# Optimization experiments

Hardware: AMD Instinct MI355X
Metric: run time of the kernel (lower is better)

The kernel has to match this reference:

```python
import jax, jax.numpy as jnp
import numpy as np

# Module hyperparameters (defaults from OrdinalPeakedCELoss.__init__)
K = 9
ALPHA = 0.4
W_FAR = 7.0
DELTA_FAR = 0.15
W_TAIL = 9.0
TAIL_POWER = 3
W_LPEAK = 12.0
PROB_MARGIN = 0.35
W_EMD = 1.2
CE_WEIGHT = 1.0
EPS = 1e-8
INV_LOGK = float(1.0 / np.log(K))
WIDTHS = np.array([3, 7, 10, 10, 10, 10, 10, 10, 25], dtype=np.float32)


def setup_inputs() -> dict:
    key = jax.random.key(0)
    k1, k2 = jax.random.split(key)
    B = 4_194_304
    logits = jax.random.normal(k1, (B, K), dtype=jnp.float32)
    y = jax.random.randint(k2, (B,), 0, K, dtype=jnp.int32)
    return {"logits": logits, "y": y}


def _loss(logits, y):
    # constant tables (tiny, [K,K])
    classes = jnp.arange(K, dtype=logits.dtype)
    d_idx = jnp.abs(classes[None, :] - classes[:, None])           # [K,K]
    tail_weights = jnp.where(d_idx > 1, (d_idx - 1.0) ** TAIL_POWER, 0.0)
    widths = jnp.asarray(WIDTHS, dtype=logits.dtype)
    cdf_weights = widths / widths.sum()                            # [K]

    # CE (class_weights are all ones -> plain NLL mean), normalized by log K
    logp = jax.nn.log_softmax(logits, axis=1)                      # [B,K]
    nll = -jnp.take_along_axis(logp, y[:, None], axis=1)[:, 0]     # [B]
    ce_loss = nll.mean() * INV_LOGK * CE_WEIGHT

    # probs: softmax, clamp_min(eps), renormalize
    probs = jax.nn.softmax(logits, axis=1)
    probs = jnp.maximum(probs, EPS)
    probs = probs / probs.sum(axis=1, keepdims=True)               # [B,K]

    py = jnp.take_along_axis(probs, y[:, None], axis=1)[:, 0]      # [B]

    # FarProbMargin: max prob among classes with |k-y|>1
    far_mask = d_idx[y] > 1                                        # [B,K]
    far_vals = jnp.where(far_mask, probs, -jnp.inf)
    far_max = jnp.max(far_vals, axis=1)
    far_max = jnp.where(jnp.isfinite(far_max), far_max, 0.0)
    far_margin = jax.nn.relu(far_max - (py - DELTA_FAR)).mean()

    # TailWeighted
    tail = (probs * tail_weights[y]).sum(axis=1).mean()            # [B] -> scalar

    # LocalPeak: neighbors y-1 / y+1 (0 when out of range)
    yl = jnp.clip(y - 1, 0, K - 1)
    yr = jnp.clip(y + 1, 0, K - 1)
    py_left = jnp.where(y > 0, jnp.take_along_axis(probs, yl[:, None], axis=1)[:, 0], 0.0)
    py_right = jnp.where(y + 1 < K, jnp.take_along_axis(probs, yr[:, None], axis=1)[:, 0], 0.0)
    neighbor_max = jnp.maximum(py_left, py_right)
    local_peak = jax.nn.relu(neighbor_max - (py - PROB_MARGIN)).mean()

    # EMD^2 over weighted CDFs
    cdf_pred = jnp.cumsum(probs, axis=1)                           # [B,K]
    cdf_true = (jnp.arange(K)[None, :] <= y[:, None]).astype(probs.dtype)
    emd2 = (((cdf_pred - cdf_true) ** 2) * cdf_weights).sum(axis=1).mean()

    ord_block = W_FAR * far_margin + W_TAIL * tail + W_LPEAK * local_peak + W_EMD * emd2
    return ce_loss + ALPHA * ord_block


def reference(logits, y):
    return _loss(logits, y)
```

## Files before the change

kernel.cpp:

```cpp
#include <hip/hip_runtime.h>
#include <math.h>

#define KC 9
#define BLOCK 256
#define RPT 512
#define NBLOCKS 2048

__device__ __forceinline__ float row_loss(const float x[KC], int yv) {
    constexpr float ALPHA = 0.4f;
    constexpr float W_FAR = 7.0f;
    constexpr float DELTA_FAR = 0.15f;
    constexpr float W_TAIL = 9.0f;
    constexpr float W_LPEAK = 12.0f;
    constexpr float PROB_MARGIN = 0.35f;
    constexpr float INV_LOGK = 0.45511961331341866f;
    constexpr float w[KC] = {3.0f/105.0f, 7.0f/105.0f, 10.0f/105.0f, 10.0f/105.0f,
                             10.0f/105.0f, 10.0f/105.0f, 10.0f/105.0f, 10.0f/105.0f,
                             25.0f/105.0f};

    float e[KC];
    float s = 0.0f;
    #pragma unroll
    for (int k = 0; k < KC; ++k) { e[k] = __expf(x[k]); s += e[k]; }
    const float inv_s = __frcp_rn(s);

    float xy = 0.0f;
    #pragma unroll
    for (int k = 0; k < KC; ++k) xy = (k == yv) ? x[k] : xy;
    const float nll = __logf(s) - xy;

    float p[KC];
    #pragma unroll
    for (int k = 0; k < KC; ++k) p[k] = e[k] * inv_s;

    float py = 0.0f, pl = 0.0f, pr = 0.0f, far_max = 0.0f, tail = 0.0f;
    float cdf = 0.0f, emd = 0.0f;
    #pragma unroll
    for (int k = 0; k < KC; ++k) {
        const int d = k - yv;
        const int ad = (d < 0) ? -d : d;
        py = (d == 0) ? p[k] : py;
        pl = (d == -1) ? p[k] : pl;
        pr = (d == 1) ? p[k] : pr;
        if (ad > 1) {
            far_max = fmaxf(far_max, p[k]);
            const float dm = (float)(ad - 1);
            tail = fmaf(p[k], dm * dm * dm, tail);
        }
        cdf += p[k];
        const float tt = (k <= yv) ? 1.0f : 0.0f;
        const float dlt = cdf - tt;
        emd = fmaf(dlt * dlt, w[k], emd);
    }

    const float far_margin = fmaxf(far_max - (py - DELTA_FAR), 0.0f);
    const float local_peak = fmaxf(fmaxf(pl, pr) - (py - PROB_MARGIN), 0.0f);

    return nll * INV_LOGK +
           ALPHA * (W_FAR * far_margin + W_TAIL * tail +
                    W_LPEAK * local_peak + 1.2f * emd);
}

__global__ __launch_bounds__(BLOCK) void ordinal_loss_kernel(
    const float* __restrict__ logits, const int* __restrict__ y,
    float* __restrict__ partials, int B, float invB)
{
    __shared__ float lds[RPT * KC];
    __shared__ float wave_sums[BLOCK / 64];

    const int t = threadIdx.x;
    const int ntiles = (B + RPT - 1) / RPT;

    float acc = 0.0f;

    for (int tile = blockIdx.x; tile < ntiles; tile += gridDim.x) {
        const int base = tile * RPT;
        const int nrows = (B - base < RPT) ? (B - base) : RPT;
        const int nflt = nrows * KC;
        const float* src = logits + (size_t)base * KC;

        const int y0 = (t < nrows) ? y[base + t] : 0;
        const int y1 = (t + BLOCK < nrows) ? y[base + t + BLOCK] : 0;

        if (nflt == RPT * KC) {
            const float4* src4 = reinterpret_cast<const float4*>(src);
            float4* lds4 = reinterpret_cast<float4*>(lds);
            lds4[t]       = src4[t];
            lds4[t + 256] = src4[t + 256];
            lds4[t + 512] = src4[t + 512];
            lds4[t + 768] = src4[t + 768];
            if (t < 128) lds4[t + 1024] = src4[t + 1024];
        } else {
            for (int i = t; i < nflt; i += BLOCK) lds[i] = src[i];
        }
        __syncthreads();

        if (t < nrows) {
            float x[KC];
            #pragma unroll
            for (int k = 0; k < KC; ++k) x[k] = lds[t * KC + k];
            acc += row_loss(x, y0);
        }
        if (t + BLOCK < nrows) {
            float x[KC];
            #pragma unroll
            for (int k = 0; k < KC; ++k) x[k] = lds[(t + BLOCK) * KC + k];
            acc += row_loss(x, y1);
        }
        __syncthreads();
    }

    float v = acc;
    #pragma unroll
    for (int off = 32; off > 0; off >>= 1) v += __shfl_down(v, off, 64);
    if ((t & 63) == 0) wave_sums[t >> 6] = v;
    __syncthreads();
    if (t == 0) {
        float bs = 0.0f;
        #pragma unroll
        for (int wv = 0; wv < BLOCK / 64; ++wv) bs += wave_sums[wv];
        partials[blockIdx.x] = bs * invB;
    }
}

__global__ __launch_bounds__(BLOCK) void reduce_kernel(
    const float* __restrict__ partials, float* __restrict__ out)
{
    __shared__ float wave_sums[BLOCK / 64];
    const int t = threadIdx.x;
    float v = 0.0f;
    #pragma unroll
    for (int j = 0; j < NBLOCKS / BLOCK; ++j) v += partials[t + j * BLOCK];
    #pragma unroll
    for (int off = 32; off > 0; off >>= 1) v += __shfl_down(v, off, 64);
    if ((t & 63) == 0) wave_sums[t >> 6] = v;
    __syncthreads();
    if (t == 0) out[0] = wave_sums[0] + wave_sums[1] + wave_sums[2] + wave_sums[3];
}

extern "C" void kernel_launch(void* const* d_in, const int* in_sizes, int n_in,
                              void* d_out, int out_size, void* d_ws, size_t ws_size,
                              hipStream_t stream) {
    const float* logits = (const float*)d_in[0];
    const int* y = (const int*)d_in[1];
    float* out = (float*)d_out;
    float* partials = (float*)d_ws;
    const int B = in_sizes[1];

    hipLaunchKernelGGL(ordinal_loss_kernel, dim3(NBLOCKS), dim3(BLOCK), 0, stream,
                       logits, y, partials, B, 1.0f / (float)B);
    hipLaunchKernelGGL(reduce_kernel, dim3(1), dim3(BLOCK), 0, stream,
                       partials, out);
}
```

Baseline: 226.5 us.

## Replace LDS-staged tile loads with direct per-thread global row loads

```diff
diff --git a/kernel.cpp b/kernel.cpp
--- a/kernel.cpp
+++ b/kernel.cpp
@@ -3,7 +3,6 @@
 
 #define KC 9
 #define BLOCK 256
-#define RPT 512
 #define NBLOCKS 2048
 
 __device__ __forceinline__ float row_loss(const float x[KC], int yv) {
@@ -65,49 +64,23 @@
     const float* __restrict__ logits, const int* __restrict__ y,
     float* __restrict__ partials, int B, float invB)
 {
-    __shared__ float lds[RPT * KC];
     __shared__ float wave_sums[BLOCK / 64];
 
     const int t = threadIdx.x;
-    const int ntiles = (B + RPT - 1) / RPT;
+    const int tid = blockIdx.x * BLOCK + t;
+    const int total = NBLOCKS * BLOCK;
 
     float acc = 0.0f;
 
-    for (int tile = blockIdx.x; tile < ntiles; tile += gridDim.x) {
-        const int base = tile * RPT;
-        const int nrows = (B - base < RPT) ? (B - base) : RPT;
-        const int nflt = nrows * KC;
-        const float* src = logits + (size_t)base * KC;
-
-        const int y0 = (t < nrows) ? y[base + t] : 0;
-        const int y1 = (t + BLOCK < nrows) ? y[base + t + BLOCK] : 0;
-
-        if (nflt == RPT * KC) {
-            const float4* src4 = reinterpret_cast<const float4*>(src);
-            float4* lds4 = reinterpret_cast<float4*>(lds);
-            lds4[t]       = src4[t];
-            lds4[t + 256] = src4[t + 256];
-            lds4[t + 512] = src4[t + 512];
-            lds4[t + 768] = src4[t + 768];
-            if (t < 128) lds4[t + 1024] = src4[t + 1024];
-        } else {
-            for (int i = t; i < nflt; i += BLOCK) lds[i] = src[i];
-        }
-        __syncthreads();
-
-        if (t < nrows) {
-            float x[KC];
-            #pragma unroll
-            for (int k = 0; k < KC; ++k) x[k] = lds[t * KC + k];
-            acc += row_loss(x, y0);
-        }
-        if (t + BLOCK < nrows) {
-            float x[KC];
-            #pragma unroll
-            for (int k = 0; k < KC; ++k) x[k] = lds[(t + BLOCK) * KC + k];
-            acc += row_loss(x, y1);
-        }
-        __syncthreads();
+    #pragma unroll 2
+    for (int r = tid; r < B; r += total) {
+        const float* row = logits + (size_t)r * KC;
+        const float4 a = *reinterpret_cast<const float4*>(row);
+        const float4 b = *reinterpret_cast<const float4*>(row + 4);
+        const float c = row[8];
+        const int yv = y[r];
+        const float x[KC] = {a.x, a.y, a.z, a.w, b.x, b.y, b.z, b.w, c};
+        acc += row_loss(x, yv);
     }
 
     float v = acc;
```

Result: no change. 223.2 us (-1.5%).
